# Optimization experiments

Hardware: AMD Instinct MI355X
Metric: run time of the kernel (lower is better)

## Reference

```python
import jax, jax.numpy as jnp
import numpy as np

B, N_EX, N_KC, D_E, D_C, D_H = 32, 1024, 128, 64, 64, 64


def setup_inputs() -> dict:
    key = jax.random.key(0)
    ks = jax.random.split(key, 20)
    return {
        "h": jax.random.normal(ks[0], (B, N_KC, D_H), jnp.float32),
        "ex": jax.random.uniform(ks[1], (B, N_EX), jnp.float32),
        "su": jax.random.uniform(ks[2], (B,), jnp.float32),
        "ex_graph": jax.random.uniform(ks[3], (N_EX, N_KC), jnp.float32),
        "kc_gamma": jax.random.normal(ks[4], (N_KC, N_KC), jnp.float32),
        "W_ex": jax.random.normal(ks[5], (D_E, 2 * N_EX), jnp.float32) * 0.02,
        "W_kc": jax.random.normal(ks[6], (D_C, N_KC), jnp.float32) * 0.05,
        "tgru_wih": jax.random.normal(ks[7], (3 * D_H, D_E), jnp.float32) * 0.05,
        "tgru_whh": jax.random.normal(ks[8], (3 * D_H, D_H), jnp.float32) * 0.05,
        "tgru_bih": jax.random.normal(ks[9], (3 * D_H,), jnp.float32) * 0.05,
        "tgru_bhh": jax.random.normal(ks[10], (3 * D_H,), jnp.float32) * 0.05,
        "fpart_w": jax.random.normal(ks[11], (D_H, D_C + D_H), jnp.float32) * 0.05,
        "fpart_b": jax.random.normal(ks[12], (D_H,), jnp.float32) * 0.05,
        "ulin_w": jax.random.normal(ks[13], (D_H, D_H), jnp.float32) * 0.05,
        "ulin_b": jax.random.normal(ks[14], (D_H,), jnp.float32) * 0.05,
        "ugru_wih": jax.random.normal(ks[15], (3 * D_H, D_H), jnp.float32) * 0.05,
        "ugru_whh": jax.random.normal(ks[16], (3 * D_H, D_H), jnp.float32) * 0.05,
        "ugru_bih": jax.random.normal(ks[17], (3 * D_H,), jnp.float32) * 0.05,
        "ugru_bhh": jax.random.normal(ks[18], (3 * D_H,), jnp.float32) * 0.05,
    }


def _gru_cell(x, h, wih, whh, bih, bhh):
    # torch.nn.GRUCell: gates in order r, z, n
    gi = x @ wih.T + bih
    gh = h @ whh.T + bhh
    ir, iz, inn = jnp.split(gi, 3, axis=-1)
    hr, hz, hn = jnp.split(gh, 3, axis=-1)
    r = jax.nn.sigmoid(ir + hr)
    z = jax.nn.sigmoid(iz + hz)
    n = jnp.tanh(inn + r * hn)
    return (1.0 - z) * n + z * h


def reference(h, ex, su, ex_graph, kc_gamma, W_ex, W_kc,
              tgru_wih, tgru_whh, tgru_bih, tgru_bhh,
              fpart_w, fpart_b, ulin_w, ulin_b,
              ugru_wih, ugru_whh, ugru_bih, ugru_bhh):
    bsz, n_kc, d_h = h.shape
    kc_graph = jax.nn.sigmoid(kc_gamma)  # (n_kc, n_kc)

    # exercise embedding from [ex*su, ex*(1-su)]
    x_id = jnp.concatenate([ex * su[:, None], ex * (1.0 - su)[:, None]], axis=-1)  # (B, 2*n_ex)
    x = x_id @ W_ex.T  # (B, d_e)

    kci = ex @ ex_graph  # (B, n_kc)
    kci_flat = kci.reshape(bsz * n_kc, 1)

    # temporal GRU update, gated by kci
    x_rep = jnp.broadcast_to(x[:, None, :], (bsz, n_kc, x.shape[-1])).reshape(bsz * n_kc, -1)
    h_flat = h.reshape(bsz * n_kc, d_h)
    th = _gru_cell(x_rep, h_flat, tgru_wih, tgru_whh, tgru_bih, tgru_bhh)
    new_h = (1.0 - kci_flat) * h_flat + kci_flat * th  # (B*n_kc, d_h)

    delta_h = (new_h - h_flat).reshape(bsz, n_kc, d_h)

    # kc_embeddings(eye(n_kc)) == W_kc.T : (n_kc, d_c)
    e = W_kc.T
    # fpart(concat([delta_h_i, e_j])) split into the two weight blocks
    W_dh = fpart_w[:, :d_h]   # acts on delta_h
    W_e = fpart_w[:, d_h:]    # acts on e
    dpart = delta_h @ W_dh.T                      # (B, n_kc_i, d_h)
    epart = e @ W_e.T + fpart_b                   # (n_kc_j, d_h)
    pre = dpart[:, :, None, :] + epart[None, None, :, :]  # (B, i, j, d_h)
    partij = jax.nn.relu(pre)
    partij = partij * kc_graph[None, :, :, None] * kci[:, :, None, None]
    partj = jnp.sum(partij, axis=1)               # (B, n_kc_j, d_h)

    outj = jax.nn.relu(partj @ ulin_w.T + ulin_b).reshape(bsz * n_kc, d_h)
    kcj = (kci @ kc_graph).reshape(bsz * n_kc, 1)

    uh = _gru_cell(outj, new_h, ugru_wih, ugru_whh, ugru_bih, ugru_bhh)
    h_out = (1.0 - kcj) * new_h + kcj * uh
    return h_out.reshape(bsz, n_kc, d_h)
```

## Files before the change

kernel.cpp:

```cpp
#include <hip/hip_runtime.h>
#include <math.h>

#define NB  32
#define NKC 128
#define DH  64
#define NEX 1024
#define G3  192

#define XOFF    0
#define KCIOFF  2048
#define NHOFF   6144
#define DPOFF   268288

__device__ __forceinline__ float sigf(float x) { return 1.0f / (1.0f + expf(-x)); }
__device__ __forceinline__ float dot4(float4 a, float4 b) {
    return fmaf(a.x, b.x, fmaf(a.y, b.y, fmaf(a.z, b.z, a.w * b.w)));
}

__global__ __launch_bounds__(256) void k0_x(
    const float* __restrict__ ex, const float* __restrict__ su,
    const float* __restrict__ W_ex, float* __restrict__ ws)
{
    int t = threadIdx.x, wave = t >> 6, lane = t & 63;
    int b = blockIdx.x >> 3;
    int dbase = (blockIdx.x & 7) * 8;
    float sub = su[b];
    const float* exb = ex + (size_t)b * NEX;
    float er[16];
    #pragma unroll
    for (int i = 0; i < 16; ++i) er[i] = exb[lane + i * 64];
    #pragma unroll
    for (int p = 0; p < 2; ++p) {
        int d = dbase + wave * 2 + p;
        const float* wr = W_ex + (size_t)d * (2 * NEX);
        float a1 = 0.f, a2 = 0.f;
        #pragma unroll
        for (int i = 0; i < 16; ++i) {
            int k = lane + i * 64;
            a1 = fmaf(er[i], wr[k], a1);
            a2 = fmaf(er[i], wr[NEX + k], a2);
        }
        float v = sub * a1 + (1.0f - sub) * a2;
        #pragma unroll
        for (int off = 32; off; off >>= 1) v += __shfl_down(v, off, 64);
        if (lane == 0) ws[XOFF + b * DH + d] = v;
    }
}

__global__ __launch_bounds__(512) void k1_tgru(
    const float* __restrict__ h, const float* __restrict__ ex,
    const float* __restrict__ ex_graph,
    const float* __restrict__ tgru_wih, const float* __restrict__ tgru_whh,
    const float* __restrict__ tgru_bih, const float* __restrict__ tgru_bhh,
    const float* __restrict__ fpart_w, float* __restrict__ ws)
{
    int t = threadIdx.x, wave = t >> 6, lane = t & 63;
    int b = blockIdx.x >> 3;
    int i0 = (blockIdx.x & 7) * 16;

    __shared__ __align__(16) float whh68[G3 * 36];
    __shared__ __align__(16) float wih68[G3 * 36];
    __shared__ __align__(16) float ht[16 * DH];
    __shared__ __align__(16) float dlt[16 * DH];
    __shared__ __align__(16) float xs[DH];
    __shared__ float kred[512];
    __shared__ float gis[G3];
    __shared__ float bhh3[G3];
    __shared__ float kciL[16];

    {
        int i = t & 15, ks = t >> 4, kb = ks * 32;
        const float* exb = ex + (size_t)b * NEX;
        const float* eg = ex_graph + i0 + i;
        float a = 0.f;
        #pragma unroll 4
        for (int k = 0; k < 32; ++k)
            a = fmaf(exb[kb + k], eg[(size_t)(kb + k) * NKC], a);
        kred[t] = a;
    }
    const float* hb = h + (size_t)(b * NKC + i0) * DH;
    for (int idx = t; idx < 16 * DH; idx += 512) ht[idx] = hb[idx];
    if (t < DH) xs[t] = ws[XOFF + b * DH + t];
    if (t < G3) bhh3[t] = tgru_bhh[t];
    __syncthreads();
    if (t < 16) {
        float s = 0.f;
        #pragma unroll
        for (int r = 0; r < 32; ++r) s += kred[r * 16 + t];
        kciL[t] = s;
        ws[KCIOFF + b * NKC + i0 + t] = s;
    }

    float giA = (t < G3) ? tgru_bih[t] : 0.f;
    float ar[2], az[2], an[2];
    #pragma unroll
    for (int m = 0; m < 2; ++m) {
        ar[m] = bhh3[lane]; az[m] = bhh3[64 + lane]; an[m] = bhh3[128 + lane];
    }
    for (int ch = 0; ch < 2; ++ch) {
        __syncthreads();
        for (int idx = t; idx < G3 * 8; idx += 512) {
            int row = idx >> 3, q = idx & 7;
            *(float4*)&whh68[row * 36 + 4 * q] =
                *(const float4*)&tgru_whh[row * DH + ch * 32 + 4 * q];
            *(float4*)&wih68[row * 36 + 4 * q] =
                *(const float4*)&tgru_wih[row * DH + ch * 32 + 4 * q];
        }
        __syncthreads();
        if (t < G3) {
            #pragma unroll
            for (int q = 0; q < 8; ++q) {
                float4 wv = *(float4*)&wih68[t * 36 + 4 * q];
                float4 xv = *(float4*)&xs[ch * 32 + 4 * q];
                giA += dot4(wv, xv);
            }
        }
        #pragma unroll
        for (int q = 0; q < 8; ++q) {
            float4 wr = *(float4*)&whh68[lane * 36 + 4 * q];
            float4 wz = *(float4*)&whh68[(64 + lane) * 36 + 4 * q];
            float4 wn = *(float4*)&whh68[(128 + lane) * 36 + 4 * q];
            int kb = ch * 32 + 4 * q;
            #pragma unroll
            for (int m = 0; m < 2; ++m) {
                float4 hk = *(float4*)&ht[(wave * 2 + m) * DH + kb];
                ar[m] += dot4(wr, hk);
                az[m] += dot4(wz, hk);
                an[m] += dot4(wn, hk);
            }
        }
    }
    if (t < G3) gis[t] = giA;
    __syncthreads();
    #pragma unroll
    for (int m = 0; m < 2; ++m) {
        int il = wave * 2 + m;
        float hval = ht[il * DH + lane];
        float r = sigf(gis[lane] + ar[m]);
        float z = sigf(gis[64 + lane] + az[m]);
        float n = tanhf(gis[128 + lane] + r * an[m]);
        float th = (1.0f - z) * n + z * hval;
        float kv = kciL[il];
        float nh = (1.0f - kv) * hval + kv * th;
        ws[NHOFF + (size_t)(b * NKC + i0 + il) * DH + lane] = nh;
        dlt[il * DH + lane] = kv * (th - hval);
    }
    __syncthreads();
    float* fw68 = whh68;
    for (int idx = t; idx < 64 * 16; idx += 512) {
        int d = idx >> 4, q = idx & 15;
        *(float4*)&fw68[d * 68 + 4 * q] = *(const float4*)&fpart_w[d * 128 + 4 * q];
    }
    __syncthreads();
    float acc[2] = {0.f, 0.f};
    #pragma unroll
    for (int q = 0; q < 16; ++q) {
        float4 w = *(float4*)&fw68[lane * 68 + 4 * q];
        #pragma unroll
        for (int m = 0; m < 2; ++m) {
            float4 dv = *(float4*)&dlt[(wave * 2 + m) * DH + 4 * q];
            acc[m] += dot4(w, dv);
        }
    }
    float* dptT = wih68;
    __syncthreads();
    #pragma unroll
    for (int m = 0; m < 2; ++m) dptT[lane * 17 + wave * 2 + m] = acc[m];
    __syncthreads();
    for (int idx = t; idx < 1024; idx += 512) {
        int d = idx >> 4, il = idx & 15;
        ws[DPOFF + (size_t)b * 8192 + d * NKC + i0 + il] = dptT[d * 17 + il];
    }
}

__global__ __launch_bounds__(512) void kB_update(
    const float* __restrict__ kc_gamma, const float* __restrict__ W_kc,
    const float* __restrict__ fpart_w, const float* __restrict__ fpart_b,
    const float* __restrict__ ulin_w, const float* __restrict__ ulin_b,
    const float* __restrict__ ugru_wih, const float* __restrict__ ugru_whh,
    const float* __restrict__ ugru_bih, const float* __restrict__ ugru_bhh,
    float* __restrict__ ws, float* __restrict__ out)
{
    int t = threadIdx.x, wave = t >> 6, lane = t & 63;
    int b = blockIdx.x >> 3;
    int j0 = (blockIdx.x & 7) * 16;

    __shared__ __align__(16) float scratch[13888];
    __shared__ __align__(16) float pjS[1024];
    __shared__ __align__(16) float outjS[1024];
    __shared__ __align__(16) float newhS[1024];
    __shared__ __align__(16) float epS[1024];
    __shared__ float kciF[NKC];
    __shared__ float kcjS[16];
    __shared__ float bihS[G3];
    __shared__ float bhhS[G3];

    float* dpT  = scratch;
    float* fw68 = scratch + 8448;
    float* wkT  = scratch + 12800;

    const float* dp = ws + DPOFF + (size_t)b * 8192;
    #pragma unroll
    for (int r = 0; r < 4; ++r) {
        int idx4 = t + r * 512;
        int d = idx4 >> 5, qi = idx4 & 31;
        *(float4*)&dpT[d * 132 + 4 * qi] = *(const float4*)&dp[d * NKC + 4 * qi];
    }
    for (int idx = t; idx < 64 * 16; idx += 512) {
        int d = idx >> 4, q = idx & 15;
        *(float4*)&fw68[d * 68 + 4 * q] =
            *(const float4*)&fpart_w[d * 128 + 64 + 4 * q];
    }
    for (int idx = t; idx < 1024; idx += 512) {
        int c = idx >> 4, jl = idx & 15;
        wkT[jl * 68 + c] = W_kc[(size_t)c * NKC + j0 + jl];
    }
    if (t < 256) {
        const float* nhp = ws + NHOFF + (size_t)(b * NKC + j0) * DH;
        *(float4*)&newhS[t * 4] = *(const float4*)&nhp[t * 4];
    }
    if (t < NKC) kciF[t] = ws[KCIOFF + b * NKC + t];
    if (t < G3) { bihS[t] = ugru_bih[t]; bhhS[t] = ugru_bhh[t]; }
    __syncthreads();
    #pragma unroll
    for (int r = 0; r < 2; ++r) {
        int idx = t + r * 512;
        int jl = idx >> 6, d = idx & 63;
        float a = fpart_b[d];
        #pragma unroll
        for (int q = 0; q < 16; ++q) {
            float4 fv = *(float4*)&fw68[d * 68 + 4 * q];
            float4 wv = *(float4*)&wkT[jl * 68 + 4 * q];
            a += dot4(fv, wv);
        }
        epS[jl * DH + d] = a;
    }
    __syncthreads();
    float* wjT = scratch + 8448;
    for (int idx = t; idx < 2048; idx += 512) {
        int i = idx >> 4, jl = idx & 15;
        wjT[jl * 132 + i] = kciF[i] * sigf(kc_gamma[i * NKC + j0 + jl]);
    }
    __syncthreads();
    if (t < 16) {
        float s = 0.f;
        #pragma unroll
        for (int qi = 0; qi < 32; ++qi) {
            float4 v = *(float4*)&wjT[t * 132 + 4 * qi];
            s += v.x + v.y + v.z + v.w;
        }
        kcjS[t] = s;
    }
    float ep[2], pa[2];
    #pragma unroll
    for (int m = 0; m < 2; ++m) {
        ep[m] = epS[(wave * 2 + m) * DH + lane]; pa[m] = 0.f;
    }
    for (int qi = 0; qi < 32; ++qi) {
        float4 dv = *(float4*)&dpT[lane * 132 + 4 * qi];
        #pragma unroll
        for (int m = 0; m < 2; ++m) {
            float4 wv = *(float4*)&wjT[(wave * 2 + m) * 132 + 4 * qi];
            pa[m] = fmaf(fmaxf(dv.x + ep[m], 0.f), wv.x, pa[m]);
            pa[m] = fmaf(fmaxf(dv.y + ep[m], 0.f), wv.y, pa[m]);
            pa[m] = fmaf(fmaxf(dv.z + ep[m], 0.f), wv.z, pa[m]);
            pa[m] = fmaf(fmaxf(dv.w + ep[m], 0.f), wv.w, pa[m]);
        }
    }
    #pragma unroll
    for (int m = 0; m < 2; ++m) pjS[(wave * 2 + m) * DH + lane] = pa[m];
    __syncthreads();
    float* ul68 = scratch;
    for (int idx = t; idx < 64 * 16; idx += 512) {
        int d = idx >> 4, q = idx & 15;
        *(float4*)&ul68[d * 68 + 4 * q] = *(const float4*)&ulin_w[d * DH + 4 * q];
    }
    float ulb = ulin_b[lane];
    __syncthreads();
    float oa[2] = {ulb, ulb};
    #pragma unroll
    for (int q = 0; q < 16; ++q) {
        float4 uv = *(float4*)&ul68[lane * 68 + 4 * q];
        #pragma unroll
        for (int m = 0; m < 2; ++m) {
            float4 pv = *(float4*)&pjS[(wave * 2 + m) * DH + 4 * q];
            oa[m] += dot4(uv, pv);
        }
    }
    #pragma unroll
    for (int m = 0; m < 2; ++m)
        outjS[(wave * 2 + m) * DH + lane] = fmaxf(oa[m], 0.f);
    float* wih36 = scratch;
    float* whh36 = scratch + 6912;
    float gir[2], giz[2], gin[2], ghr[2], ghz[2], ghn[2];
    #pragma unroll
    for (int m = 0; m < 2; ++m)
        gir[m] = giz[m] = gin[m] = ghr[m] = ghz[m] = ghn[m] = 0.f;
    for (int ch = 0; ch < 2; ++ch) {
        __syncthreads();
        for (int idx = t; idx < G3 * 8; idx += 512) {
            int row = idx >> 3, q = idx & 7;
            *(float4*)&wih36[row * 36 + 4 * q] =
                *(const float4*)&ugru_wih[row * DH + ch * 32 + 4 * q];
            *(float4*)&whh36[row * 36 + 4 * q] =
                *(const float4*)&ugru_whh[row * DH + ch * 32 + 4 * q];
        }
        __syncthreads();
        #pragma unroll
        for (int q = 0; q < 8; ++q) {
            float4 wir = *(float4*)&wih36[lane * 36 + 4 * q];
            float4 wiz = *(float4*)&wih36[(64 + lane) * 36 + 4 * q];
            float4 win = *(float4*)&wih36[(128 + lane) * 36 + 4 * q];
            float4 wwr = *(float4*)&whh36[lane * 36 + 4 * q];
            float4 wwz = *(float4*)&whh36[(64 + lane) * 36 + 4 * q];
            float4 wwn = *(float4*)&whh36[(128 + lane) * 36 + 4 * q];
            int kb = ch * 32 + 4 * q;
            #pragma unroll
            for (int m = 0; m < 2; ++m) {
                int jl = wave * 2 + m;
                float4 ov = *(float4*)&outjS[jl * DH + kb];
                float4 nv = *(float4*)&newhS[jl * DH + kb];
                gir[m] += dot4(wir, ov);
                giz[m] += dot4(wiz, ov);
                gin[m] += dot4(win, ov);
                ghr[m] += dot4(wwr, nv);
                ghz[m] += dot4(wwz, nv);
                ghn[m] += dot4(wwn, nv);
            }
        }
    }
    #pragma unroll
    for (int m = 0; m < 2; ++m) {
        int jl = wave * 2 + m;
        float r = sigf(gir[m] + bihS[lane] + ghr[m] + bhhS[lane]);
        float z = sigf(giz[m] + bihS[64 + lane] + ghz[m] + bhhS[64 + lane]);
        float n = tanhf(gin[m] + bihS[128 + lane] + r * (ghn[m] + bhhS[128 + lane]));
        float nh = newhS[jl * DH + lane];
        float uh = (1.0f - z) * n + z * nh;
        float kj = kcjS[jl];
        out[(size_t)(b * NKC + j0 + jl) * DH + lane] = (1.0f - kj) * nh + kj * uh;
    }
}

extern "C" void kernel_launch(void* const* d_in, const int* in_sizes, int n_in,
                              void* d_out, int out_size, void* d_ws, size_t ws_size,
                              hipStream_t stream) {
    const float* h        = (const float*)d_in[0];
    const float* ex       = (const float*)d_in[1];
    const float* su       = (const float*)d_in[2];
    const float* ex_graph = (const float*)d_in[3];
    const float* kc_gamma = (const float*)d_in[4];
    const float* W_ex     = (const float*)d_in[5];
    const float* W_kc     = (const float*)d_in[6];
    const float* tgru_wih = (const float*)d_in[7];
    const float* tgru_whh = (const float*)d_in[8];
    const float* tgru_bih = (const float*)d_in[9];
    const float* tgru_bhh = (const float*)d_in[10];
    const float* fpart_w  = (const float*)d_in[11];
    const float* fpart_b  = (const float*)d_in[12];
    const float* ulin_w   = (const float*)d_in[13];
    const float* ulin_b   = (const float*)d_in[14];
    const float* ugru_wih = (const float*)d_in[15];
    const float* ugru_whh = (const float*)d_in[16];
    const float* ugru_bih = (const float*)d_in[17];
    const float* ugru_bhh = (const float*)d_in[18];
    float* ws  = (float*)d_ws;
    float* out = (float*)d_out;

    hipLaunchKernelGGL(k0_x, dim3(256), dim3(256), 0, stream,
                       ex, su, W_ex, ws);
    hipLaunchKernelGGL(k1_tgru, dim3(256), dim3(512), 0, stream,
                       h, ex, ex_graph, tgru_wih, tgru_whh, tgru_bih,
                       tgru_bhh, fpart_w, ws);
    hipLaunchKernelGGL(kB_update, dim3(256), dim3(512), 0, stream,
                       kc_gamma, W_kc, fpart_w, fpart_b, ulin_w, ulin_b,
                       ugru_wih, ugru_whh, ugru_bih, ugru_bhh, ws, out);
}
```

Before: 128.1 us.

## Fuse three kernels into one with per-batch atomic flag barriers

Merges the x-projection, temporal GRU and update kernels into a single persistent kernel. Each group of 8 blocks sharing a batch index synchronises through global atomic counters with spin-waits, and new_h stays in shared memory instead of going through workspace. This removes two kernel launch boundaries and a global round trip, at the cost of an extra memset launch. It also relies on all 256 blocks being co-resident, or at least all 8 blocks of each batch, to avoid deadlock.

```diff
diff --git a/kernel.cpp b/kernel.cpp
--- a/kernel.cpp
+++ b/kernel.cpp
@@ -9,29 +9,66 @@
 
 #define XOFF    0
 #define KCIOFF  2048
-#define NHOFF   6144
-#define DPOFF   268288
+#define DPOFF   6144
+#define FLAGOFF 268288
+#define FLAGBYTE (FLAGOFF * 4)
+
+#define S_WHH   0
+#define S_WIH   6912
+#define S_HT    13824
+#define S_DLT   14848
+#define S_XS    15872
+#define S_KRED  15936
+#define S_GIS   16448
+#define S_BHH3  16640
+#define S_KCIL  16832
+#define S_DPT   0
+#define S_FWB   8448
+#define S_WKT   12800
+#define S_PJS   13888
+#define S_OUTJ  14912
+#define S_EPS   15936
+#define S_NEWH  17024
+#define S_KCIF  18048
+#define S_KCJ   18176
+#define S_BIH   18192
+#define S_BHH   18384
+#define SM_SIZE 18576
 
 __device__ __forceinline__ float sigf(float x) { return 1.0f / (1.0f + expf(-x)); }
 __device__ __forceinline__ float dot4(float4 a, float4 b) {
     return fmaf(a.x, b.x, fmaf(a.y, b.y, fmaf(a.z, b.z, a.w * b.w)));
 }
 
-__global__ __launch_bounds__(256) void k0_x(
-    const float* __restrict__ ex, const float* __restrict__ su,
-    const float* __restrict__ W_ex, float* __restrict__ ws)
+__global__ __launch_bounds__(512) void kF(
+    const float* __restrict__ h, const float* __restrict__ ex,
+    const float* __restrict__ su, const float* __restrict__ ex_graph,
+    const float* __restrict__ kc_gamma,
+    const float* __restrict__ W_ex, const float* __restrict__ W_kc,
+    const float* __restrict__ tgru_wih, const float* __restrict__ tgru_whh,
+    const float* __restrict__ tgru_bih, const float* __restrict__ tgru_bhh,
+    const float* __restrict__ fpart_w, const float* __restrict__ fpart_b,
+    const float* __restrict__ ulin_w, const float* __restrict__ ulin_b,
+    const float* __restrict__ ugru_wih, const float* __restrict__ ugru_whh,
+    const float* __restrict__ ugru_bih, const float* __restrict__ ugru_bhh,
+    float* __restrict__ ws, float* __restrict__ out)
 {
     int t = threadIdx.x, wave = t >> 6, lane = t & 63;
-    int b = blockIdx.x >> 3;
-    int dbase = (blockIdx.x & 7) * 8;
-    float sub = su[b];
-    const float* exb = ex + (size_t)b * NEX;
-    float er[16];
-    #pragma unroll
-    for (int i = 0; i < 16; ++i) er[i] = exb[lane + i * 64];
-    #pragma unroll
-    for (int p = 0; p < 2; ++p) {
-        int d = dbase + wave * 2 + p;
+    int b  = blockIdx.x >> 3;
+    int ck = blockIdx.x & 7;
+    int i0 = ck * 16;
+
+    __shared__ __align__(16) float sm[SM_SIZE];
+    int* fx = (int*)(ws + FLAGOFF);
+    int* fd = fx + 32;
+
+    {
+        float sub = su[b];
+        const float* exb = ex + (size_t)b * NEX;
+        float er[16];
+        #pragma unroll
+        for (int i = 0; i < 16; ++i) er[i] = exb[lane + i * 64];
+        int d = ck * 8 + wave;
         const float* wr = W_ex + (size_t)d * (2 * NEX);
         float a1 = 0.f, a2 = 0.f;
         #pragma unroll
@@ -45,28 +82,9 @@
         for (int off = 32; off; off >>= 1) v += __shfl_down(v, off, 64);
         if (lane == 0) ws[XOFF + b * DH + d] = v;
     }
-}
-
-__global__ __launch_bounds__(512) void k1_tgru(
-    const float* __restrict__ h, const float* __restrict__ ex,
-    const float* __restrict__ ex_graph,
-    const float* __restrict__ tgru_wih, const float* __restrict__ tgru_whh,
-    const float* __restrict__ tgru_bih, const float* __restrict__ tgru_bhh,
-    const float* __restrict__ fpart_w, float* __restrict__ ws)
-{
-    int t = threadIdx.x, wave = t >> 6, lane = t & 63;
-    int b = blockIdx.x >> 3;
-    int i0 = (blockIdx.x & 7) * 16;
-
-    __shared__ __align__(16) float whh68[G3 * 36];
-    __shared__ __align__(16) float wih68[G3 * 36];
-    __shared__ __align__(16) float ht[16 * DH];
-    __shared__ __align__(16) float dlt[16 * DH];
-    __shared__ __align__(16) float xs[DH];
-    __shared__ float kred[512];
-    __shared__ float gis[G3];
-    __shared__ float bhh3[G3];
-    __shared__ float kciL[16];
+    __syncthreads();
+    if (t == 0)
+        __hip_atomic_fetch_add(fx + b, 1, __ATOMIC_RELEASE, __HIP_MEMORY_SCOPE_AGENT);
 
     {
         int i = t & 15, ks = t >> 4, kb = ks * 32;
@@ -76,151 +94,137 @@
         #pragma unroll 4
         for (int k = 0; k < 32; ++k)
             a = fmaf(exb[kb + k], eg[(size_t)(kb + k) * NKC], a);
-        kred[t] = a;
-    }
-    const float* hb = h + (size_t)(b * NKC + i0) * DH;
-    for (int idx = t; idx < 16 * DH; idx += 512) ht[idx] = hb[idx];
-    if (t < DH) xs[t] = ws[XOFF + b * DH + t];
-    if (t < G3) bhh3[t] = tgru_bhh[t];
+        sm[S_KRED + t] = a;
+    }
+    {
+        const float* hb = h + (size_t)(b * NKC + i0) * DH;
+        for (int idx = t; idx < 16 * DH; idx += 512) sm[S_HT + idx] = hb[idx];
+    }
+    if (t < G3) sm[S_BHH3 + t] = tgru_bhh[t];
     __syncthreads();
     if (t < 16) {
         float s = 0.f;
         #pragma unroll
-        for (int r = 0; r < 32; ++r) s += kred[r * 16 + t];
-        kciL[t] = s;
+        for (int r = 0; r < 32; ++r) s += sm[S_KRED + r * 16 + t];
+        sm[S_KCIL + t] = s;
         ws[KCIOFF + b * NKC + i0 + t] = s;
     }
+    if (t == 0) {
+        while (__hip_atomic_load(fx + b, __ATOMIC_ACQUIRE, __HIP_MEMORY_SCOPE_AGENT) < 8)
+            __builtin_amdgcn_s_sleep(1);
+    }
+    __syncthreads();
+    if (t < DH) sm[S_XS + t] = ws[XOFF + b * DH + t];
 
     float giA = (t < G3) ? tgru_bih[t] : 0.f;
     float ar[2], az[2], an[2];
     #pragma unroll
     for (int m = 0; m < 2; ++m) {
-        ar[m] = bhh3[lane]; az[m] = bhh3[64 + lane]; an[m] = bhh3[128 + lane];
+        ar[m] = sm[S_BHH3 + lane];
+        az[m] = sm[S_BHH3 + 64 + lane];
+        an[m] = sm[S_BHH3 + 128 + lane];
     }
     for (int ch = 0; ch < 2; ++ch) {
         __syncthreads();
         for (int idx = t; idx < G3 * 8; idx += 512) {
             int row = idx >> 3, q = idx & 7;
-            *(float4*)&whh68[row * 36 + 4 * q] =
+            *(float4*)&sm[S_WHH + row * 36 + 4 * q] =
                 *(const float4*)&tgru_whh[row * DH + ch * 32 + 4 * q];
-            *(float4*)&wih68[row * 36 + 4 * q] =
+            *(float4*)&sm[S_WIH + row * 36 + 4 * q] =
                 *(const float4*)&tgru_wih[row * DH + ch * 32 + 4 * q];
         }
         __syncthreads();
         if (t < G3) {
             #pragma unroll
             for (int q = 0; q < 8; ++q) {
-                float4 wv = *(float4*)&wih68[t * 36 + 4 * q];
-                float4 xv = *(float4*)&xs[ch * 32 + 4 * q];
+                float4 wv = *(float4*)&sm[S_WIH + t * 36 + 4 * q];
+                float4 xv = *(float4*)&sm[S_XS + ch * 32 + 4 * q];
                 giA += dot4(wv, xv);
             }
         }
         #pragma unroll
         for (int q = 0; q < 8; ++q) {
-            float4 wr = *(float4*)&whh68[lane * 36 + 4 * q];
-            float4 wz = *(float4*)&whh68[(64 + lane) * 36 + 4 * q];
-            float4 wn = *(float4*)&whh68[(128 + lane) * 36 + 4 * q];
-            int kb = ch * 32 + 4 * q;
+            float4 wr = *(float4*)&sm[S_WHH + lane * 36 + 4 * q];
+            float4 wz = *(float4*)&sm[S_WHH + (64 + lane) * 36 + 4 * q];
+            float4 wn = *(float4*)&sm[S_WHH + (128 + lane) * 36 + 4 * q];
+            int kb2 = ch * 32 + 4 * q;
             #pragma unroll
             for (int m = 0; m < 2; ++m) {
-                float4 hk = *(float4*)&ht[(wave * 2 + m) * DH + kb];
+                float4 hk = *(float4*)&sm[S_HT + (wave * 2 + m) * DH + kb2];
                 ar[m] += dot4(wr, hk);
                 az[m] += dot4(wz, hk);
                 an[m] += dot4(wn, hk);
             }
         }
     }
-    if (t < G3) gis[t] = giA;
+    if (t < G3) sm[S_GIS + t] = giA;
     __syncthreads();
     #pragma unroll
     for (int m = 0; m < 2; ++m) {
         int il = wave * 2 + m;
-        float hval = ht[il * DH + lane];
-        float r = sigf(gis[lane] + ar[m]);
-        float z = sigf(gis[64 + lane] + az[m]);
-        float n = tanhf(gis[128 + lane] + r * an[m]);
+        float hval = sm[S_HT + il * DH + lane];
+        float r = sigf(sm[S_GIS + lane] + ar[m]);
+        float z = sigf(sm[S_GIS + 64 + lane] + az[m]);
+        float n = tanhf(sm[S_GIS + 128 + lane] + r * an[m]);
         float th = (1.0f - z) * n + z * hval;
-        float kv = kciL[il];
+        float kv = sm[S_KCIL + il];
         float nh = (1.0f - kv) * hval + kv * th;
-        ws[NHOFF + (size_t)(b * NKC + i0 + il) * DH + lane] = nh;
-        dlt[il * DH + lane] = kv * (th - hval);
-    }
-    __syncthreads();
-    float* fw68 = whh68;
+        sm[S_NEWH + il * DH + lane] = nh;
+        sm[S_DLT + il * DH + lane] = kv * (th - hval);
+    }
+    __syncthreads();
     for (int idx = t; idx < 64 * 16; idx += 512) {
         int d = idx >> 4, q = idx & 15;
-        *(float4*)&fw68[d * 68 + 4 * q] = *(const float4*)&fpart_w[d * 128 + 4 * q];
+        *(float4*)&sm[S_WHH + d * 68 + 4 * q] = *(const float4*)&fpart_w[d * 128 + 4 * q];
     }
     __syncthreads();
     float acc[2] = {0.f, 0.f};
     #pragma unroll
     for (int q = 0; q < 16; ++q) {
-        float4 w = *(float4*)&fw68[lane * 68 + 4 * q];
+        float4 w = *(float4*)&sm[S_WHH + lane * 68 + 4 * q];
         #pragma unroll
         for (int m = 0; m < 2; ++m) {
-            float4 dv = *(float4*)&dlt[(wave * 2 + m) * DH + 4 * q];
+            float4 dv = *(float4*)&sm[S_DLT + (wave * 2 + m) * DH + 4 * q];
             acc[m] += dot4(w, dv);
         }
     }
-    float* dptT = wih68;
-    __syncthreads();
-    #pragma unroll
-    for (int m = 0; m < 2; ++m) dptT[lane * 17 + wave * 2 + m] = acc[m];
+    __syncthreads();
+    #pragma unroll
+    for (int m = 0; m < 2; ++m) sm[S_WIH + lane * 17 + wave * 2 + m] = acc[m];
     __syncthreads();
     for (int idx = t; idx < 1024; idx += 512) {
         int d = idx >> 4, il = idx & 15;
-        ws[DPOFF + (size_t)b * 8192 + d * NKC + i0 + il] = dptT[d * 17 + il];
-    }
-}
-
-__global__ __launch_bounds__(512) void kB_update(
-    const float* __restrict__ kc_gamma, const float* __restrict__ W_kc,
-    const float* __restrict__ fpart_w, const float* __restrict__ fpart_b,
-    const float* __restrict__ ulin_w, const float* __restrict__ ulin_b,
-    const float* __restrict__ ugru_wih, const float* __restrict__ ugru_whh,
-    const float* __restrict__ ugru_bih, const float* __restrict__ ugru_bhh,
-    float* __restrict__ ws, float* __restrict__ out)
-{
-    int t = threadIdx.x, wave = t >> 6, lane = t & 63;
-    int b = blockIdx.x >> 3;
-    int j0 = (blockIdx.x & 7) * 16;
-
-    __shared__ __align__(16) float scratch[13888];
-    __shared__ __align__(16) float pjS[1024];
-    __shared__ __align__(16) float outjS[1024];
-    __shared__ __align__(16) float newhS[1024];
-    __shared__ __align__(16) float epS[1024];
-    __shared__ float kciF[NKC];
-    __shared__ float kcjS[16];
-    __shared__ float bihS[G3];
-    __shared__ float bhhS[G3];
-
-    float* dpT  = scratch;
-    float* fw68 = scratch + 8448;
-    float* wkT  = scratch + 12800;
-
-    const float* dp = ws + DPOFF + (size_t)b * 8192;
-    #pragma unroll
-    for (int r = 0; r < 4; ++r) {
-        int idx4 = t + r * 512;
-        int d = idx4 >> 5, qi = idx4 & 31;
-        *(float4*)&dpT[d * 132 + 4 * qi] = *(const float4*)&dp[d * NKC + 4 * qi];
-    }
+        ws[DPOFF + (size_t)b * 8192 + d * NKC + i0 + il] = sm[S_WIH + d * 17 + il];
+    }
+    __syncthreads();
+    if (t == 0)
+        __hip_atomic_fetch_add(fd + b, 1, __ATOMIC_RELEASE, __HIP_MEMORY_SCOPE_AGENT);
+
     for (int idx = t; idx < 64 * 16; idx += 512) {
         int d = idx >> 4, q = idx & 15;
-        *(float4*)&fw68[d * 68 + 4 * q] =
+        *(float4*)&sm[S_FWB + d * 68 + 4 * q] =
             *(const float4*)&fpart_w[d * 128 + 64 + 4 * q];
     }
     for (int idx = t; idx < 1024; idx += 512) {
-        int c = idx >> 4, jl = idx & 15;
-        wkT[jl * 68 + c] = W_kc[(size_t)c * NKC + j0 + jl];
-    }
-    if (t < 256) {
-        const float* nhp = ws + NHOFF + (size_t)(b * NKC + j0) * DH;
-        *(float4*)&newhS[t * 4] = *(const float4*)&nhp[t * 4];
-    }
-    if (t < NKC) kciF[t] = ws[KCIOFF + b * NKC + t];
-    if (t < G3) { bihS[t] = ugru_bih[t]; bhhS[t] = ugru_bhh[t]; }
+        int cc = idx >> 4, jl = idx & 15;
+        sm[S_WKT + jl * 68 + cc] = W_kc[(size_t)cc * NKC + i0 + jl];
+    }
+    if (t < G3) { sm[S_BIH + t] = ugru_bih[t]; sm[S_BHH + t] = ugru_bhh[t]; }
+    if (t == 0) {
+        while (__hip_atomic_load(fd + b, __ATOMIC_ACQUIRE, __HIP_MEMORY_SCOPE_AGENT) < 8)
+            __builtin_amdgcn_s_sleep(1);
+    }
+    __syncthreads();
+    {
+        const float* dp = ws + DPOFF + (size_t)b * 8192;
+        #pragma unroll
+        for (int r = 0; r < 4; ++r) {
+            int idx4 = t + r * 512;
+            int d = idx4 >> 5, qi = idx4 & 31;
+            *(float4*)&sm[S_DPT + d * 132 + 4 * qi] = *(const float4*)&dp[d * NKC + 4 * qi];
+        }
+    }
+    if (t < NKC) sm[S_KCIF + t] = ws[KCIOFF + b * NKC + t];
     __syncthreads();
     #pragma unroll
     for (int r = 0; r < 2; ++r) {
@@ -229,38 +233,38 @@
         float a = fpart_b[d];
         #pragma unroll
         for (int q = 0; q < 16; ++q) {
-            float4 fv = *(float4*)&fw68[d * 68 + 4 * q];
-            float4 wv = *(float4*)&wkT[jl * 68 + 4 * q];
+            float4 fv = *(float4*)&sm[S_FWB + d * 68 + 4 * q];
+            float4 wv = *(float4*)&sm[S_WKT + jl * 68 + 4 * q];
             a += dot4(fv, wv);
         }
-        epS[jl * DH + d] = a;
-    }
-    __syncthreads();
-    float* wjT = scratch + 8448;
+        sm[S_EPS + jl * DH + d] = a;
+    }
+    __syncthreads();
     for (int idx = t; idx < 2048; idx += 512) {
         int i = idx >> 4, jl = idx & 15;
-        wjT[jl * 132 + i] = kciF[i] * sigf(kc_gamma[i * NKC + j0 + jl]);
+        sm[S_FWB + jl * 132 + i] = sm[S_KCIF + i] * sigf(kc_gamma[i * NKC + i0 + jl]);
     }
     __syncthreads();
     if (t < 16) {
         float s = 0.f;
         #pragma unroll
         for (int qi = 0; qi < 32; ++qi) {
-            float4 v = *(float4*)&wjT[t * 132 + 4 * qi];
+            float4 v = *(float4*)&sm[S_FWB + t * 132 + 4 * qi];
             s += v.x + v.y + v.z + v.w;
         }
-        kcjS[t] = s;
+        sm[S_KCJ + t] = s;
     }
     float ep[2], pa[2];
     #pragma unroll
     for (int m = 0; m < 2; ++m) {
-        ep[m] = epS[(wave * 2 + m) * DH + lane]; pa[m] = 0.f;
+        ep[m] = sm[S_EPS + (wave * 2 + m) * DH + lane];
+        pa[m] = 0.f;
     }
     for (int qi = 0; qi < 32; ++qi) {
-        float4 dv = *(float4*)&dpT[lane * 132 + 4 * qi];
+        float4 dv = *(float4*)&sm[S_DPT + lane * 132 + 4 * qi];
         #pragma unroll
         for (int m = 0; m < 2; ++m) {
-            float4 wv = *(float4*)&wjT[(wave * 2 + m) * 132 + 4 * qi];
+            float4 wv = *(float4*)&sm[S_FWB + (wave * 2 + m) * 132 + 4 * qi];
             pa[m] = fmaf(fmaxf(dv.x + ep[m], 0.f), wv.x, pa[m]);
             pa[m] = fmaf(fmaxf(dv.y + ep[m], 0.f), wv.y, pa[m]);
             pa[m] = fmaf(fmaxf(dv.z + ep[m], 0.f), wv.z, pa[m]);
@@ -268,30 +272,27 @@
         }
     }
     #pragma unroll
-    for (int m = 0; m < 2; ++m) pjS[(wave * 2 + m) * DH + lane] = pa[m];
-    __syncthreads();
-    float* ul68 = scratch;
+    for (int m = 0; m < 2; ++m) sm[S_PJS + (wave * 2 + m) * DH + lane] = pa[m];
+    __syncthreads();
     for (int idx = t; idx < 64 * 16; idx += 512) {
         int d = idx >> 4, q = idx & 15;
-        *(float4*)&ul68[d * 68 + 4 * q] = *(const float4*)&ulin_w[d * DH + 4 * q];
+        *(float4*)&sm[d * 68 + 4 * q] = *(const float4*)&ulin_w[d * DH + 4 * q];
     }
     float ulb = ulin_b[lane];
     __syncthreads();
     float oa[2] = {ulb, ulb};
     #pragma unroll
     for (int q = 0; q < 16; ++q) {
-        float4 uv = *(float4*)&ul68[lane * 68 + 4 * q];
+        float4 uv = *(float4*)&sm[lane * 68 + 4 * q];
         #pragma unroll
         for (int m = 0; m < 2; ++m) {
-            float4 pv = *(float4*)&pjS[(wave * 2 + m) * DH + 4 * q];
+            float4 pv = *(float4*)&sm[S_PJS + (wave * 2 + m) * DH + 4 * q];
             oa[m] += dot4(uv, pv);
         }
     }
     #pragma unroll
     for (int m = 0; m < 2; ++m)
-        outjS[(wave * 2 + m) * DH + lane] = fmaxf(oa[m], 0.f);
-    float* wih36 = scratch;
-    float* whh36 = scratch + 6912;
+        sm[S_OUTJ + (wave * 2 + m) * DH + lane] = fmaxf(oa[m], 0.f);
     float gir[2], giz[2], gin[2], ghr[2], ghz[2], ghn[2];
     #pragma unroll
     for (int m = 0; m < 2; ++m)
@@ -300,26 +301,26 @@
         __syncthreads();
         for (int idx = t; idx < G3 * 8; idx += 512) {
             int row = idx >> 3, q = idx & 7;
-            *(float4*)&wih36[row * 36 + 4 * q] =
+            *(float4*)&sm[row * 36 + 4 * q] =
                 *(const float4*)&ugru_wih[row * DH + ch * 32 + 4 * q];
-            *(float4*)&whh36[row * 36 + 4 * q] =
+            *(float4*)&sm[6912 + row * 36 + 4 * q] =
                 *(const float4*)&ugru_whh[row * DH + ch * 32 + 4 * q];
         }
         __syncthreads();
         #pragma unroll
         for (int q = 0; q < 8; ++q) {
-            float4 wir = *(float4*)&wih36[lane * 36 + 4 * q];
-            float4 wiz = *(float4*)&wih36[(64 + lane) * 36 + 4 * q];
-            float4 win = *(float4*)&wih36[(128 + lane) * 36 + 4 * q];
-            float4 wwr = *(float4*)&whh36[lane * 36 + 4 * q];
-            float4 wwz = *(float4*)&whh36[(64 + lane) * 36 + 4 * q];
-            float4 wwn = *(float4*)&whh36[(128 + lane) * 36 + 4 * q];
-            int kb = ch * 32 + 4 * q;
+            float4 wir = *(float4*)&sm[lane * 36 + 4 * q];
+            float4 wiz = *(float4*)&sm[(64 + lane) * 36 + 4 * q];
+            float4 win = *(float4*)&sm[(128 + lane) * 36 + 4 * q];
+            float4 wwr = *(float4*)&sm[6912 + lane * 36 + 4 * q];
+            float4 wwz = *(float4*)&sm[6912 + (64 + lane) * 36 + 4 * q];
+            float4 wwn = *(float4*)&sm[6912 + (128 + lane) * 36 + 4 * q];
+            int kb2 = ch * 32 + 4 * q;
             #pragma unroll
             for (int m = 0; m < 2; ++m) {
                 int jl = wave * 2 + m;
-                float4 ov = *(float4*)&outjS[jl * DH + kb];
-                float4 nv = *(float4*)&newhS[jl * DH + kb];
+                float4 ov = *(float4*)&sm[S_OUTJ + jl * DH + kb2];
+                float4 nv = *(float4*)&sm[S_NEWH + jl * DH + kb2];
                 gir[m] += dot4(wir, ov);
                 giz[m] += dot4(wiz, ov);
                 gin[m] += dot4(win, ov);
@@ -332,13 +333,14 @@
     #pragma unroll
     for (int m = 0; m < 2; ++m) {
         int jl = wave * 2 + m;
-        float r = sigf(gir[m] + bihS[lane] + ghr[m] + bhhS[lane]);
-        float z = sigf(giz[m] + bihS[64 + lane] + ghz[m] + bhhS[64 + lane]);
-        float n = tanhf(gin[m] + bihS[128 + lane] + r * (ghn[m] + bhhS[128 + lane]));
-        float nh = newhS[jl * DH + lane];
+        float r = sigf(gir[m] + sm[S_BIH + lane] + ghr[m] + sm[S_BHH + lane]);
+        float z = sigf(giz[m] + sm[S_BIH + 64 + lane] + ghz[m] + sm[S_BHH + 64 + lane]);
+        float n = tanhf(gin[m] + sm[S_BIH + 128 + lane] +
+                        r * (ghn[m] + sm[S_BHH + 128 + lane]));
+        float nh = sm[S_NEWH + jl * DH + lane];
         float uh = (1.0f - z) * n + z * nh;
-        float kj = kcjS[jl];
-        out[(size_t)(b * NKC + j0 + jl) * DH + lane] = (1.0f - kj) * nh + kj * uh;
+        float kj = sm[S_KCJ + jl];
+        out[(size_t)(b * NKC + i0 + jl) * DH + lane] = (1.0f - kj) * nh + kj * uh;
     }
 }
 
@@ -367,12 +369,11 @@
     float* ws  = (float*)d_ws;
     float* out = (float*)d_out;
 
-    hipLaunchKernelGGL(k0_x, dim3(256), dim3(256), 0, stream,
-                       ex, su, W_ex, ws);
-    hipLaunchKernelGGL(k1_tgru, dim3(256), dim3(512), 0, stream,
-                       h, ex, ex_graph, tgru_wih, tgru_whh, tgru_bih,
-                       tgru_bhh, fpart_w, ws);
-    hipLaunchKernelGGL(kB_update, dim3(256), dim3(512), 0, stream,
-                       kc_gamma, W_kc, fpart_w, fpart_b, ulin_w, ulin_b,
-                       ugru_wih, ugru_whh, ugru_bih, ugru_bhh, ws, out);
+    hipMemsetAsync((char*)d_ws + FLAGBYTE, 0, 64 * sizeof(int), stream);
+    hipLaunchKernelGGL(kF, dim3(256), dim3(512), 0, stream,
+                       h, ex, su, ex_graph, kc_gamma, W_ex, W_kc,
+                       tgru_wih, tgru_whh, tgru_bih, tgru_bhh,
+                       fpart_w, fpart_b, ulin_w, ulin_b,
+                       ugru_wih, ugru_whh, ugru_bih, ugru_bhh,
+                       ws, out);
 }
```

After: 134.6 us. 1.05x slower.

## Reschedule weight staging and drop shared transposes in GRU/update kernels

Applied to the files above, without the earlier changes.

In the GRU kernel the first weight chunk is loaded before the kci reduction, the h tile load is vectorised, and the delta-part output is written straight to global memory instead of being transposed through shared memory. In the update kernel shared memory is packed into one buffer with overlapping regions. The ulin and GRU weight loads are issued earlier so they overlap other work, and delta-part rows are read from global memory rather than staged in a padded shared tile. Several unroll pragmas are reduced. These changes aim to cut synchronisations and LDS footprint for better occupancy, at the cost of uncoalesced global stores and loads for the dp array.

```diff
diff --git a/kernel.cpp b/kernel.cpp
--- a/kernel.cpp
+++ b/kernel.cpp
@@ -1,7 +1,6 @@
 #include <hip/hip_runtime.h>
 #include <math.h>
 
-#define NB  32
 #define NKC 128
 #define DH  64
 #define NEX 1024
@@ -34,7 +33,7 @@
         int d = dbase + wave * 2 + p;
         const float* wr = W_ex + (size_t)d * (2 * NEX);
         float a1 = 0.f, a2 = 0.f;
-        #pragma unroll
+        #pragma unroll 8
         for (int i = 0; i < 16; ++i) {
             int k = lane + i * 64;
             a1 = fmaf(er[i], wr[k], a1);
@@ -68,6 +67,13 @@
     __shared__ float bhh3[G3];
     __shared__ float kciL[16];
 
+    for (int idx = t; idx < G3 * 8; idx += 512) {
+        int row = idx >> 3, q = idx & 7;
+        *(float4*)&whh68[row * 36 + 4 * q] =
+            *(const float4*)&tgru_whh[row * DH + 4 * q];
+        *(float4*)&wih68[row * 36 + 4 * q] =
+            *(const float4*)&tgru_wih[row * DH + 4 * q];
+    }
     {
         int i = t & 15, ks = t >> 4, kb = ks * 32;
         const float* exb = ex + (size_t)b * NEX;
@@ -78,8 +84,10 @@
             a = fmaf(exb[kb + k], eg[(size_t)(kb + k) * NKC], a);
         kred[t] = a;
     }
-    const float* hb = h + (size_t)(b * NKC + i0) * DH;
-    for (int idx = t; idx < 16 * DH; idx += 512) ht[idx] = hb[idx];
+    if (t < 256) {
+        const float* hb = h + (size_t)(b * NKC + i0) * DH;
+        *(float4*)&ht[t * 4] = *(const float4*)&hb[t * 4];
+    }
     if (t < DH) xs[t] = ws[XOFF + b * DH + t];
     if (t < G3) bhh3[t] = tgru_bhh[t];
     __syncthreads();
@@ -97,37 +105,50 @@
     for (int m = 0; m < 2; ++m) {
         ar[m] = bhh3[lane]; az[m] = bhh3[64 + lane]; an[m] = bhh3[128 + lane];
     }
-    for (int ch = 0; ch < 2; ++ch) {
-        __syncthreads();
-        for (int idx = t; idx < G3 * 8; idx += 512) {
-            int row = idx >> 3, q = idx & 7;
-            *(float4*)&whh68[row * 36 + 4 * q] =
-                *(const float4*)&tgru_whh[row * DH + ch * 32 + 4 * q];
-            *(float4*)&wih68[row * 36 + 4 * q] =
-                *(const float4*)&tgru_wih[row * DH + ch * 32 + 4 * q];
-        }
-        __syncthreads();
-        if (t < G3) {
-            #pragma unroll
-            for (int q = 0; q < 8; ++q) {
-                float4 wv = *(float4*)&wih68[t * 36 + 4 * q];
-                float4 xv = *(float4*)&xs[ch * 32 + 4 * q];
-                giA += dot4(wv, xv);
-            }
-        }
-        #pragma unroll
-        for (int q = 0; q < 8; ++q) {
-            float4 wr = *(float4*)&whh68[lane * 36 + 4 * q];
-            float4 wz = *(float4*)&whh68[(64 + lane) * 36 + 4 * q];
-            float4 wn = *(float4*)&whh68[(128 + lane) * 36 + 4 * q];
-            int kb = ch * 32 + 4 * q;
-            #pragma unroll
-            for (int m = 0; m < 2; ++m) {
-                float4 hk = *(float4*)&ht[(wave * 2 + m) * DH + kb];
-                ar[m] += dot4(wr, hk);
-                az[m] += dot4(wz, hk);
-                an[m] += dot4(wn, hk);
-            }
+    if (t < G3) {
+        #pragma unroll 4
+        for (int q = 0; q < 8; ++q)
+            giA += dot4(*(float4*)&wih68[t * 36 + 4 * q], *(float4*)&xs[4 * q]);
+    }
+    #pragma unroll 4
+    for (int q = 0; q < 8; ++q) {
+        float4 wr_ = *(float4*)&whh68[lane * 36 + 4 * q];
+        float4 wz_ = *(float4*)&whh68[(64 + lane) * 36 + 4 * q];
+        float4 wn_ = *(float4*)&whh68[(128 + lane) * 36 + 4 * q];
+        #pragma unroll
+        for (int m = 0; m < 2; ++m) {
+            float4 hk = *(float4*)&ht[(wave * 2 + m) * DH + 4 * q];
+            ar[m] += dot4(wr_, hk);
+            az[m] += dot4(wz_, hk);
+            an[m] += dot4(wn_, hk);
+        }
+    }
+    __syncthreads();
+    for (int idx = t; idx < G3 * 8; idx += 512) {
+        int row = idx >> 3, q = idx & 7;
+        *(float4*)&whh68[row * 36 + 4 * q] =
+            *(const float4*)&tgru_whh[row * DH + 32 + 4 * q];
+        *(float4*)&wih68[row * 36 + 4 * q] =
+            *(const float4*)&tgru_wih[row * DH + 32 + 4 * q];
+    }
+    __syncthreads();
+    if (t < G3) {
+        #pragma unroll 4
+        for (int q = 0; q < 8; ++q)
+            giA += dot4(*(float4*)&wih68[t * 36 + 4 * q], *(float4*)&xs[32 + 4 * q]);
+    }
+    #pragma unroll 4
+    for (int q = 0; q < 8; ++q) {
+        int kb2 = 32 + 4 * q;
+        float4 wr_ = *(float4*)&whh68[lane * 36 + 4 * q];
+        float4 wz_ = *(float4*)&whh68[(64 + lane) * 36 + 4 * q];
+        float4 wn_ = *(float4*)&whh68[(128 + lane) * 36 + 4 * q];
+        #pragma unroll
+        for (int m = 0; m < 2; ++m) {
+            float4 hk = *(float4*)&ht[(wave * 2 + m) * DH + kb2];
+            ar[m] += dot4(wr_, hk);
+            az[m] += dot4(wz_, hk);
+            an[m] += dot4(wn_, hk);
         }
     }
     if (t < G3) gis[t] = giA;
@@ -153,25 +174,32 @@
     }
     __syncthreads();
     float acc[2] = {0.f, 0.f};
-    #pragma unroll
+    #pragma unroll 4
     for (int q = 0; q < 16; ++q) {
         float4 w = *(float4*)&fw68[lane * 68 + 4 * q];
         #pragma unroll
-        for (int m = 0; m < 2; ++m) {
-            float4 dv = *(float4*)&dlt[(wave * 2 + m) * DH + 4 * q];
-            acc[m] += dot4(w, dv);
-        }
-    }
-    float* dptT = wih68;
-    __syncthreads();
-    #pragma unroll
-    for (int m = 0; m < 2; ++m) dptT[lane * 17 + wave * 2 + m] = acc[m];
-    __syncthreads();
-    for (int idx = t; idx < 1024; idx += 512) {
-        int d = idx >> 4, il = idx & 15;
-        ws[DPOFF + (size_t)b * 8192 + d * NKC + i0 + il] = dptT[d * 17 + il];
-    }
+        for (int m = 0; m < 2; ++m)
+            acc[m] += dot4(w, *(float4*)&dlt[(wave * 2 + m) * DH + 4 * q]);
+    }
+    float* dpb = ws + DPOFF + (size_t)b * 8192 + (size_t)lane * NKC + i0;
+    #pragma unroll
+    for (int m = 0; m < 2; ++m) dpb[wave * 2 + m] = acc[m];
 }
+
+#define KB_FWB   0
+#define KB_WKT   4352
+#define KB_WIH36 0
+#define KB_UL    6912
+#define KB_PJS   11264
+#define KB_WHH36 6912
+#define KB_WJT   13824
+#define KB_OUTJ  15936
+#define KB_NEWH  16960
+#define KB_KCIF  17984
+#define KB_KCJ   18112
+#define KB_BIH   18128
+#define KB_BHH   18320
+#define KB_SM    18512
 
 __global__ __launch_bounds__(512) void kB_update(
     const float* __restrict__ kc_gamma, const float* __restrict__ W_kc,
@@ -185,159 +213,166 @@
     int b = blockIdx.x >> 3;
     int j0 = (blockIdx.x & 7) * 16;
 
-    __shared__ __align__(16) float scratch[13888];
-    __shared__ __align__(16) float pjS[1024];
-    __shared__ __align__(16) float outjS[1024];
-    __shared__ __align__(16) float newhS[1024];
-    __shared__ __align__(16) float epS[1024];
-    __shared__ float kciF[NKC];
-    __shared__ float kcjS[16];
-    __shared__ float bihS[G3];
-    __shared__ float bhhS[G3];
-
-    float* dpT  = scratch;
-    float* fw68 = scratch + 8448;
-    float* wkT  = scratch + 12800;
-
-    const float* dp = ws + DPOFF + (size_t)b * 8192;
-    #pragma unroll
-    for (int r = 0; r < 4; ++r) {
-        int idx4 = t + r * 512;
-        int d = idx4 >> 5, qi = idx4 & 31;
-        *(float4*)&dpT[d * 132 + 4 * qi] = *(const float4*)&dp[d * NKC + 4 * qi];
-    }
-    for (int idx = t; idx < 64 * 16; idx += 512) {
+    __shared__ __align__(16) float sm[KB_SM];
+
+    for (int idx = t; idx < 1024; idx += 512) {
         int d = idx >> 4, q = idx & 15;
-        *(float4*)&fw68[d * 68 + 4 * q] =
+        *(float4*)&sm[KB_FWB + d * 68 + 4 * q] =
             *(const float4*)&fpart_w[d * 128 + 64 + 4 * q];
+        *(float4*)&sm[KB_UL + d * 68 + 4 * q] =
+            *(const float4*)&ulin_w[d * DH + 4 * q];
     }
     for (int idx = t; idx < 1024; idx += 512) {
         int c = idx >> 4, jl = idx & 15;
-        wkT[jl * 68 + c] = W_kc[(size_t)c * NKC + j0 + jl];
+        sm[KB_WKT + jl * 68 + c] = W_kc[(size_t)c * NKC + j0 + jl];
     }
     if (t < 256) {
         const float* nhp = ws + NHOFF + (size_t)(b * NKC + j0) * DH;
-        *(float4*)&newhS[t * 4] = *(const float4*)&nhp[t * 4];
-    }
-    if (t < NKC) kciF[t] = ws[KCIOFF + b * NKC + t];
-    if (t < G3) { bihS[t] = ugru_bih[t]; bhhS[t] = ugru_bhh[t]; }
-    __syncthreads();
-    #pragma unroll
-    for (int r = 0; r < 2; ++r) {
-        int idx = t + r * 512;
-        int jl = idx >> 6, d = idx & 63;
-        float a = fpart_b[d];
-        #pragma unroll
-        for (int q = 0; q < 16; ++q) {
-            float4 fv = *(float4*)&fw68[d * 68 + 4 * q];
-            float4 wv = *(float4*)&wkT[jl * 68 + 4 * q];
-            a += dot4(fv, wv);
-        }
-        epS[jl * DH + d] = a;
-    }
-    __syncthreads();
-    float* wjT = scratch + 8448;
+        *(float4*)&sm[KB_NEWH + t * 4] = *(const float4*)&nhp[t * 4];
+    }
+    if (t < NKC) sm[KB_KCIF + t] = ws[KCIOFF + b * NKC + t];
+    if (t < G3) { sm[KB_BIH + t] = ugru_bih[t]; sm[KB_BHH + t] = ugru_bhh[t]; }
+    float fpb = fpart_b[lane];
+    float ulb = ulin_b[lane];
+    __syncthreads();
+
+    float epv[2];
+    #pragma unroll
+    for (int m = 0; m < 2; ++m) {
+        float a = fpb;
+        #pragma unroll 4
+        for (int q = 0; q < 16; ++q)
+            a += dot4(*(float4*)&sm[KB_FWB + lane * 68 + 4 * q],
+                      *(float4*)&sm[KB_WKT + (wave * 2 + m) * 68 + 4 * q]);
+        epv[m] = a;
+    }
     for (int idx = t; idx < 2048; idx += 512) {
         int i = idx >> 4, jl = idx & 15;
-        wjT[jl * 132 + i] = kciF[i] * sigf(kc_gamma[i * NKC + j0 + jl]);
+        sm[KB_WJT + jl * 132 + i] =
+            sm[KB_KCIF + i] * sigf(kc_gamma[(size_t)i * NKC + j0 + jl]);
     }
     __syncthreads();
     if (t < 16) {
         float s = 0.f;
-        #pragma unroll
+        #pragma unroll 8
         for (int qi = 0; qi < 32; ++qi) {
-            float4 v = *(float4*)&wjT[t * 132 + 4 * qi];
+            float4 v = *(float4*)&sm[KB_WJT + t * 132 + 4 * qi];
             s += v.x + v.y + v.z + v.w;
         }
-        kcjS[t] = s;
-    }
-    float ep[2], pa[2];
-    #pragma unroll
-    for (int m = 0; m < 2; ++m) {
-        ep[m] = epS[(wave * 2 + m) * DH + lane]; pa[m] = 0.f;
-    }
-    for (int qi = 0; qi < 32; ++qi) {
-        float4 dv = *(float4*)&dpT[lane * 132 + 4 * qi];
-        #pragma unroll
-        for (int m = 0; m < 2; ++m) {
-            float4 wv = *(float4*)&wjT[(wave * 2 + m) * 132 + 4 * qi];
-            pa[m] = fmaf(fmaxf(dv.x + ep[m], 0.f), wv.x, pa[m]);
-            pa[m] = fmaf(fmaxf(dv.y + ep[m], 0.f), wv.y, pa[m]);
-            pa[m] = fmaf(fmaxf(dv.z + ep[m], 0.f), wv.z, pa[m]);
-            pa[m] = fmaf(fmaxf(dv.w + ep[m], 0.f), wv.w, pa[m]);
-        }
-    }
-    #pragma unroll
-    for (int m = 0; m < 2; ++m) pjS[(wave * 2 + m) * DH + lane] = pa[m];
-    __syncthreads();
-    float* ul68 = scratch;
-    for (int idx = t; idx < 64 * 16; idx += 512) {
-        int d = idx >> 4, q = idx & 15;
-        *(float4*)&ul68[d * 68 + 4 * q] = *(const float4*)&ulin_w[d * DH + 4 * q];
-    }
-    float ulb = ulin_b[lane];
+        sm[KB_KCJ + t] = s;
+    }
+    for (int idx = t; idx < G3 * 8; idx += 512) {
+        int row = idx >> 3, q = idx & 7;
+        *(float4*)&sm[KB_WIH36 + row * 36 + 4 * q] =
+            *(const float4*)&ugru_wih[row * DH + 4 * q];
+    }
+    {
+        const float* dprow = ws + DPOFF + (size_t)b * 8192 + (size_t)lane * NKC;
+        float pa0 = 0.f, pa1 = 0.f;
+        float ep0 = epv[0], ep1 = epv[1];
+        #pragma unroll 8
+        for (int qi = 0; qi < 32; ++qi) {
+            float4 dv = *(const float4*)&dprow[4 * qi];
+            float4 w0 = *(float4*)&sm[KB_WJT + (wave * 2 + 0) * 132 + 4 * qi];
+            float4 w1 = *(float4*)&sm[KB_WJT + (wave * 2 + 1) * 132 + 4 * qi];
+            pa0 = fmaf(fmaxf(dv.x + ep0, 0.f), w0.x, pa0);
+            pa0 = fmaf(fmaxf(dv.y + ep0, 0.f), w0.y, pa0);
+            pa0 = fmaf(fmaxf(dv.z + ep0, 0.f), w0.z, pa0);
+            pa0 = fmaf(fmaxf(dv.w + ep0, 0.f), w0.w, pa0);
+            pa1 = fmaf(fmaxf(dv.x + ep1, 0.f), w1.x, pa1);
+            pa1 = fmaf(fmaxf(dv.y + ep1, 0.f), w1.y, pa1);
+            pa1 = fmaf(fmaxf(dv.z + ep1, 0.f), w1.z, pa1);
+            pa1 = fmaf(fmaxf(dv.w + ep1, 0.f), w1.w, pa1);
+        }
+        sm[KB_PJS + (wave * 2 + 0) * DH + lane] = pa0;
+        sm[KB_PJS + (wave * 2 + 1) * DH + lane] = pa1;
+    }
     __syncthreads();
     float oa[2] = {ulb, ulb};
-    #pragma unroll
+    #pragma unroll 4
     for (int q = 0; q < 16; ++q) {
-        float4 uv = *(float4*)&ul68[lane * 68 + 4 * q];
-        #pragma unroll
-        for (int m = 0; m < 2; ++m) {
-            float4 pv = *(float4*)&pjS[(wave * 2 + m) * DH + 4 * q];
-            oa[m] += dot4(uv, pv);
-        }
+        float4 uv = *(float4*)&sm[KB_UL + lane * 68 + 4 * q];
+        #pragma unroll
+        for (int m = 0; m < 2; ++m)
+            oa[m] += dot4(uv, *(float4*)&sm[KB_PJS + (wave * 2 + m) * DH + 4 * q]);
     }
     #pragma unroll
     for (int m = 0; m < 2; ++m)
-        outjS[(wave * 2 + m) * DH + lane] = fmaxf(oa[m], 0.f);
-    float* wih36 = scratch;
-    float* whh36 = scratch + 6912;
+        sm[KB_OUTJ + (wave * 2 + m) * DH + lane] = fmaxf(oa[m], 0.f);
+    __syncthreads();
+    for (int idx = t; idx < G3 * 8; idx += 512) {
+        int row = idx >> 3, q = idx & 7;
+        *(float4*)&sm[KB_WHH36 + row * 36 + 4 * q] =
+            *(const float4*)&ugru_whh[row * DH + 4 * q];
+    }
+    __syncthreads();
     float gir[2], giz[2], gin[2], ghr[2], ghz[2], ghn[2];
     #pragma unroll
     for (int m = 0; m < 2; ++m)
         gir[m] = giz[m] = gin[m] = ghr[m] = ghz[m] = ghn[m] = 0.f;
-    for (int ch = 0; ch < 2; ++ch) {
-        __syncthreads();
-        for (int idx = t; idx < G3 * 8; idx += 512) {
-            int row = idx >> 3, q = idx & 7;
-            *(float4*)&wih36[row * 36 + 4 * q] =
-                *(const float4*)&ugru_wih[row * DH + ch * 32 + 4 * q];
-            *(float4*)&whh36[row * 36 + 4 * q] =
-                *(const float4*)&ugru_whh[row * DH + ch * 32 + 4 * q];
-        }
-        __syncthreads();
-        #pragma unroll
-        for (int q = 0; q < 8; ++q) {
-            float4 wir = *(float4*)&wih36[lane * 36 + 4 * q];
-            float4 wiz = *(float4*)&wih36[(64 + lane) * 36 + 4 * q];
-            float4 win = *(float4*)&wih36[(128 + lane) * 36 + 4 * q];
-            float4 wwr = *(float4*)&whh36[lane * 36 + 4 * q];
-            float4 wwz = *(float4*)&whh36[(64 + lane) * 36 + 4 * q];
-            float4 wwn = *(float4*)&whh36[(128 + lane) * 36 + 4 * q];
-            int kb = ch * 32 + 4 * q;
-            #pragma unroll
-            for (int m = 0; m < 2; ++m) {
-                int jl = wave * 2 + m;
-                float4 ov = *(float4*)&outjS[jl * DH + kb];
-                float4 nv = *(float4*)&newhS[jl * DH + kb];
-                gir[m] += dot4(wir, ov);
-                giz[m] += dot4(wiz, ov);
-                gin[m] += dot4(win, ov);
-                ghr[m] += dot4(wwr, nv);
-                ghz[m] += dot4(wwz, nv);
-                ghn[m] += dot4(wwn, nv);
-            }
+    #pragma unroll 2
+    for (int q = 0; q < 8; ++q) {
+        int kb2 = 4 * q;
+        float4 wir = *(float4*)&sm[KB_WIH36 + lane * 36 + 4 * q];
+        float4 wiz = *(float4*)&sm[KB_WIH36 + (64 + lane) * 36 + 4 * q];
+        float4 win = *(float4*)&sm[KB_WIH36 + (128 + lane) * 36 + 4 * q];
+        float4 wwr = *(float4*)&sm[KB_WHH36 + lane * 36 + 4 * q];
+        float4 wwz = *(float4*)&sm[KB_WHH36 + (64 + lane) * 36 + 4 * q];
+        float4 wwn = *(float4*)&sm[KB_WHH36 + (128 + lane) * 36 + 4 * q];
+        #pragma unroll
+        for (int m = 0; m < 2; ++m) {
+            int jl = wave * 2 + m;
+            float4 ov = *(float4*)&sm[KB_OUTJ + jl * DH + kb2];
+            float4 nv = *(float4*)&sm[KB_NEWH + jl * DH + kb2];
+            gir[m] += dot4(wir, ov);
+            giz[m] += dot4(wiz, ov);
+            gin[m] += dot4(win, ov);
+            ghr[m] += dot4(wwr, nv);
+            ghz[m] += dot4(wwz, nv);
+            ghn[m] += dot4(wwn, nv);
+        }
+    }
+    __syncthreads();
+    for (int idx = t; idx < G3 * 8; idx += 512) {
+        int row = idx >> 3, q = idx & 7;
+        *(float4*)&sm[KB_WIH36 + row * 36 + 4 * q] =
+            *(const float4*)&ugru_wih[row * DH + 32 + 4 * q];
+        *(float4*)&sm[KB_WHH36 + row * 36 + 4 * q] =
+            *(const float4*)&ugru_whh[row * DH + 32 + 4 * q];
+    }
+    __syncthreads();
+    #pragma unroll 2
+    for (int q = 0; q < 8; ++q) {
+        int kb2 = 32 + 4 * q;
+        float4 wir = *(float4*)&sm[KB_WIH36 + lane * 36 + 4 * q];
+        float4 wiz = *(float4*)&sm[KB_WIH36 + (64 + lane) * 36 + 4 * q];
+        float4 win = *(float4*)&sm[KB_WIH36 + (128 + lane) * 36 + 4 * q];
+        float4 wwr = *(float4*)&sm[KB_WHH36 + lane * 36 + 4 * q];
+        float4 wwz = *(float4*)&sm[KB_WHH36 + (64 + lane) * 36 + 4 * q];
+        float4 wwn = *(float4*)&sm[KB_WHH36 + (128 + lane) * 36 + 4 * q];
+        #pragma unroll
+        for (int m = 0; m < 2; ++m) {
+            int jl = wave * 2 + m;
+            float4 ov = *(float4*)&sm[KB_OUTJ + jl * DH + kb2];
+            float4 nv = *(float4*)&sm[KB_NEWH + jl * DH + kb2];
+            gir[m] += dot4(wir, ov);
+            giz[m] += dot4(wiz, ov);
+            gin[m] += dot4(win, ov);
+            ghr[m] += dot4(wwr, nv);
+            ghz[m] += dot4(wwz, nv);
+            ghn[m] += dot4(wwn, nv);
         }
     }
     #pragma unroll
     for (int m = 0; m < 2; ++m) {
         int jl = wave * 2 + m;
-        float r = sigf(gir[m] + bihS[lane] + ghr[m] + bhhS[lane]);
-        float z = sigf(giz[m] + bihS[64 + lane] + ghz[m] + bhhS[64 + lane]);
-        float n = tanhf(gin[m] + bihS[128 + lane] + r * (ghn[m] + bhhS[128 + lane]));
-        float nh = newhS[jl * DH + lane];
+        float r = sigf(gir[m] + sm[KB_BIH + lane] + ghr[m] + sm[KB_BHH + lane]);
+        float z = sigf(giz[m] + sm[KB_BIH + 64 + lane] + ghz[m] + sm[KB_BHH + 64 + lane]);
+        float n = tanhf(gin[m] + sm[KB_BIH + 128 + lane] +
+                        r * (ghn[m] + sm[KB_BHH + 128 + lane]));
+        float nh = sm[KB_NEWH + jl * DH + lane];
         float uh = (1.0f - z) * n + z * nh;
-        float kj = kcjS[jl];
+        float kj = sm[KB_KCJ + jl];
         out[(size_t)(b * NKC + j0 + jl) * DH + lane] = (1.0f - kj) * nh + kj * uh;
     }
 }
```

After: 128.2 us. About the same (+0.1%).
